# Performance work log

Hardware: AMD Instinct MI355X
Metric: run time of the kernel (lower is better)

The kernel has to match this reference:

```python
import jax, jax.numpy as jnp
import numpy as np

B, S, H, N = 2, 2048, 512, 64


def setup_inputs() -> dict:
    key = jax.random.key(0)
    ks = jax.random.split(key, 8)
    da_input = jax.random.normal(ks[0], (B, S, H), dtype=jnp.float32)
    # per-(batch, timestep) scalar time step; kept >= 4 so exp(delta*A) is stable
    da_orky_delta = jax.random.uniform(ks[1], (B, S), dtype=jnp.float32, minval=4.0, maxval=5.0)
    # all-negative A so the elementwise exp(delta*A) recurrence stays bounded
    A = -(jnp.abs(jax.random.normal(ks[2], (N, N), dtype=jnp.float32)) * 0.5 + 2.0)
    B_w = jax.random.normal(ks[3], (N, H), dtype=jnp.float32) * (1.0 / np.sqrt(H))
    C_w = jax.random.normal(ks[4], (H, N), dtype=jnp.float32) * (1.0 / np.sqrt(N))
    C_b = jax.random.normal(ks[5], (H,), dtype=jnp.float32) * 0.01
    D_w = jax.random.normal(ks[6], (H, H), dtype=jnp.float32) * (1.0 / np.sqrt(H))
    D_b = jax.random.normal(ks[7], (H,), dtype=jnp.float32) * 0.01
    return {"da_input": da_input, "da_orky_delta": da_orky_delta,
            "A": A, "B_w": B_w, "C_w": C_w, "C_b": C_b, "D_w": D_w, "D_b": D_b}


def _ssm_forward(da_input, da_orky_delta, A, B_w, C_w, C_b, D_w, D_b):
    Bsz, Slen, Hdim = da_input.shape
    Ndim = A.shape[0]
    # --- discretization: A_bar = exp(delta * A) (elementwise, as in torch.exp)
    A_bar = jnp.exp(da_orky_delta[:, :, None, None] * A)          # (B,S,N,N)
    I = jnp.eye(Ndim, dtype=A.dtype)
    A_inv = jnp.linalg.inv(A)                                      # (N,N)
    # B_bar = (A_bar - I) @ A^{-1} @ B_w  -> (B,S,N,H)
    B_bar = jnp.einsum('bsmn,nk,kh->bsmh', A_bar - I, A_inv, B_w)
    # per-step input projection: x_t @ B_bar_t^T  -> (B,S,N)
    inp_proj = jnp.einsum('bsh,bsnh->bsn', da_input, B_bar)

    # --- sequential selective scan: h_t = h_{t-1} @ A_bar_t + u_t
    def step(h, xs):
        Abar_t, u_t = xs                                           # (B,N,N), (B,N)
        h = jnp.einsum('bm,bmn->bn', h, Abar_t) + u_t
        return h, h

    h0 = jnp.zeros((Bsz, Ndim), dtype=da_input.dtype)
    _, hs = jax.lax.scan(step, h0, (jnp.swapaxes(A_bar, 0, 1), jnp.swapaxes(inp_proj, 0, 1)))
    hs = jnp.swapaxes(hs, 0, 1)                                    # (B,S,N)

    # y_t = C(h_t) + D(x_t)
    y = (jnp.einsum('bsn,hn->bsh', hs, C_w) + C_b
         + jnp.einsum('bsh,gh->bsg', da_input, D_w) + D_b)
    return y


def reference(da_input, da_orky_delta, A, B_w, C_w, C_b, D_w, D_b):
    return _ssm_forward(da_input, da_orky_delta, A, B_w, C_w, C_b, D_w, D_b)
```

## Files before the change

### kernel.cpp

```cpp
#include <hip/hip_runtime.h>
#include <hip/hip_bf16.h>

#define BSZ 2
#define SLEN 2048
#define HDIM 512
#define NDIM 64
#define TTOT (BSZ * SLEN)

#define CHUNK_L 4
#define HALO_K 3

typedef short bf16x8 __attribute__((ext_vector_type(8)));
typedef unsigned short u16x8 __attribute__((ext_vector_type(8)));
typedef float f32x4 __attribute__((ext_vector_type(4)));

__device__ inline unsigned short f2b(float f) {
    unsigned u = __float_as_uint(f);
    return (unsigned short)((u + 0x7FFFu + ((u >> 16) & 1u)) >> 16);
}
__device__ inline float b2f(unsigned short b) {
    return __uint_as_float(((unsigned)b) << 16);
}

__global__ __launch_bounds__(256) void k_pre(const float* __restrict__ A,
                                             const float* __restrict__ X,
                                             const float* __restrict__ Dw,
                                             const float* __restrict__ Bw,
                                             const float* __restrict__ Cb,
                                             const float* __restrict__ Db,
                                             float* __restrict__ Ainv,
                                             unsigned short* __restrict__ Vws,
                                             float* __restrict__ Y) {
    __shared__ float colb0[2][64], colb1[2][64];
    __shared__ float4 rowb0[2][16], rowb1[2][16];
    __shared__ unsigned short Xs[64][72];
    __shared__ unsigned short Ws[64][72];

    if (blockIdx.x == 0) {
        const int tid = threadIdx.x;
        const int r = tid >> 2;
        const int c = tid & 3;

        float4 q0, q1, q2, q3;
        {
            const float4* A4 = (const float4*)(A + (size_t)r * 64 + c * 16);
            q0 = A4[0]; q1 = A4[1]; q2 = A4[2]; q3 = A4[3];
        }

        for (int kb = 0; kb < 32; ++kb) {
            const int k0 = 2 * kb, k1 = k0 + 1;
            const int par = kb & 1;
            if (c == (k0 >> 4)) {
                int sel2 = (k0 & 15) >> 1;
                float v0 = q0.x, v1 = q0.y;
                if (sel2 == 1) { v0 = q0.z; v1 = q0.w; }
                if (sel2 == 2) { v0 = q1.x; v1 = q1.y; }
                if (sel2 == 3) { v0 = q1.z; v1 = q1.w; }
                if (sel2 == 4) { v0 = q2.x; v1 = q2.y; }
                if (sel2 == 5) { v0 = q2.z; v1 = q2.w; }
                if (sel2 == 6) { v0 = q3.x; v1 = q3.y; }
                if (sel2 == 7) { v0 = q3.z; v1 = q3.w; }
                colb0[par][r] = v0; colb1[par][r] = v1;
            }
            if (r == k0) {
                rowb0[par][c * 4 + 0] = q0; rowb0[par][c * 4 + 1] = q1;
                rowb0[par][c * 4 + 2] = q2; rowb0[par][c * 4 + 3] = q3;
            }
            if (r == k1) {
                rowb1[par][c * 4 + 0] = q0; rowb1[par][c * 4 + 1] = q1;
                rowb1[par][c * 4 + 2] = q2; rowb1[par][c * 4 + 3] = q3;
            }
            __syncthreads();

            float a00 = colb0[par][k0], a01 = colb1[par][k0];
            float a10 = colb0[par][k1], a11 = colb1[par][k1];
            float idet = 1.0f / (a00 * a11 - a01 * a10);
            float d00 = a11 * idet, d01 = -a01 * idet;
            float d10 = -a10 * idet, d11 = a00 * idet;

            float f0 = colb0[par][r], f1 = colb1[par][r];
            bool isp0 = (r == k0), isp1 = (r == k1);
            float g0 = f0 * d00 + f1 * d10;
            float g1 = f0 * d01 + f1 * d11;
            float al0 = isp0 ? d00 : (isp1 ? d10 : -g0);
            float al1 = isp0 ? d01 : (isp1 ? d11 : -g1);
            float beta = (isp0 || isp1) ? 0.0f : 1.0f;

            float4 p0q0 = rowb0[par][c * 4 + 0], p0q1 = rowb0[par][c * 4 + 1];
            float4 p0q2 = rowb0[par][c * 4 + 2], p0q3 = rowb0[par][c * 4 + 3];
            float4 p1q0 = rowb1[par][c * 4 + 0], p1q1 = rowb1[par][c * 4 + 1];
            float4 p1q2 = rowb1[par][c * 4 + 2], p1q3 = rowb1[par][c * 4 + 3];
            int selk = k0 - c * 16;

            #define UPD2(Q, P0, P1) { \
                float4 mv = q##Q; \
                float4 nv; \
                nv.x = fmaf(al0, P0.x, fmaf(al1, P1.x, beta * mv.x)); \
                nv.y = fmaf(al0, P0.y, fmaf(al1, P1.y, beta * mv.y)); \
                nv.z = fmaf(al0, P0.z, fmaf(al1, P1.z, beta * mv.z)); \
                nv.w = fmaf(al0, P0.w, fmaf(al1, P1.w, beta * mv.w)); \
                if (4 * (Q) + 0 == selk) { nv.x = al0; nv.y = al1; } \
                if (4 * (Q) + 2 == selk) { nv.z = al0; nv.w = al1; } \
                q##Q = nv; \
            }
            UPD2(0, p0q0, p1q0)
            UPD2(1, p0q1, p1q1)
            UPD2(2, p0q2, p1q2)
            UPD2(3, p0q3, p1q3)
        }

        float4* O = (float4*)(Ainv + (size_t)r * 64 + c * 16);
        O[0] = q0; O[1] = q1; O[2] = q2; O[3] = q3;
        return;
    }

    int tid = threadIdx.x;
    int wv = tid >> 6, lane = tid & 63;
    int sr = tid >> 2;
    int sc = (tid & 3) * 16;
    const int arow = wv * 16 + (lane & 15);
    const int akof = (lane >> 4) * 8;

    if (blockIdx.x <= 512) {
        int bid = blockIdx.x - 1;
        int t0 = (bid >> 3) * 64, h0 = (bid & 7) * 64;

        f32x4 acc0 = {0.f, 0.f, 0.f, 0.f}, acc1 = acc0, acc2 = acc0, acc3 = acc0;

        for (int st = 0; st < 8; ++st) {
            int k0 = st * 64;
            __syncthreads();
            {
                const float4* xp = (const float4*)&X[(size_t)(t0 + sr) * 512 + k0 + sc];
                const float4* wp = (const float4*)&Dw[(size_t)(h0 + sr) * 512 + k0 + sc];
                float4 x0 = xp[0], x1 = xp[1], x2 = xp[2], x3 = xp[3];
                float4 w0 = wp[0], w1 = wp[1], w2 = wp[2], w3 = wp[3];
                u16x8 a0 = {f2b(x0.x), f2b(x0.y), f2b(x0.z), f2b(x0.w),
                            f2b(x1.x), f2b(x1.y), f2b(x1.z), f2b(x1.w)};
                u16x8 a1 = {f2b(x2.x), f2b(x2.y), f2b(x2.z), f2b(x2.w),
                            f2b(x3.x), f2b(x3.y), f2b(x3.z), f2b(x3.w)};
                u16x8 b0 = {f2b(w0.x), f2b(w0.y), f2b(w0.z), f2b(w0.w),
                            f2b(w1.x), f2b(w1.y), f2b(w1.z), f2b(w1.w)};
                u16x8 b1 = {f2b(w2.x), f2b(w2.y), f2b(w2.z), f2b(w2.w),
                            f2b(w3.x), f2b(w3.y), f2b(w3.z), f2b(w3.w)};
                *(u16x8*)&Xs[sr][sc] = a0; *(u16x8*)&Xs[sr][sc + 8] = a1;
                *(u16x8*)&Ws[sr][sc] = b0; *(u16x8*)&Ws[sr][sc + 8] = b1;
            }
            __syncthreads();
            #pragma unroll
            for (int ks = 0; ks < 2; ++ks) {
                bf16x8 a = *(const bf16x8*)&Xs[arow][ks * 32 + akof];
                bf16x8 b0 = *(const bf16x8*)&Ws[0 * 16 + (lane & 15)][ks * 32 + akof];
                bf16x8 b1 = *(const bf16x8*)&Ws[1 * 16 + (lane & 15)][ks * 32 + akof];
                bf16x8 b2 = *(const bf16x8*)&Ws[2 * 16 + (lane & 15)][ks * 32 + akof];
                bf16x8 b3 = *(const bf16x8*)&Ws[3 * 16 + (lane & 15)][ks * 32 + akof];
                acc0 = __builtin_amdgcn_mfma_f32_16x16x32_bf16(a, b0, acc0, 0, 0, 0);
                acc1 = __builtin_amdgcn_mfma_f32_16x16x32_bf16(a, b1, acc1, 0, 0, 0);
                acc2 = __builtin_amdgcn_mfma_f32_16x16x32_bf16(a, b2, acc2, 0, 0, 0);
                acc3 = __builtin_amdgcn_mfma_f32_16x16x32_bf16(a, b3, acc3, 0, 0, 0);
            }
        }

        int rbase = t0 + wv * 16 + (lane >> 4) * 4;
        #define EPI(f, accv) { \
            int col = h0 + (f) * 16 + (lane & 15); \
            float bias = Cb[col] + Db[col]; \
            Y[(size_t)(rbase + 0) * 512 + col] = accv[0] + bias; \
            Y[(size_t)(rbase + 1) * 512 + col] = accv[1] + bias; \
            Y[(size_t)(rbase + 2) * 512 + col] = accv[2] + bias; \
            Y[(size_t)(rbase + 3) * 512 + col] = accv[3] + bias; \
        }
        EPI(0, acc0) EPI(1, acc1) EPI(2, acc2) EPI(3, acc3)
        return;
    }

    {
        int bidv = blockIdx.x - 513;
        int t0 = bidv * 64;

        f32x4 acc0 = {0.f, 0.f, 0.f, 0.f}, acc1 = acc0, acc2 = acc0, acc3 = acc0;

        for (int st = 0; st < 8; ++st) {
            int k0 = st * 64;
            __syncthreads();
            {
                const float4* xp = (const float4*)&X[(size_t)(t0 + sr) * 512 + k0 + sc];
                const float4* bp = (const float4*)&Bw[(size_t)sr * 512 + k0 + sc];
                float4 x0 = xp[0], x1 = xp[1], x2 = xp[2], x3 = xp[3];
                float4 w0 = bp[0], w1 = bp[1], w2 = bp[2], w3 = bp[3];
                u16x8 a0 = {f2b(x0.x), f2b(x0.y), f2b(x0.z), f2b(x0.w),
                            f2b(x1.x), f2b(x1.y), f2b(x1.z), f2b(x1.w)};
                u16x8 a1 = {f2b(x2.x), f2b(x2.y), f2b(x2.z), f2b(x2.w),
                            f2b(x3.x), f2b(x3.y), f2b(x3.z), f2b(x3.w)};
                u16x8 b0 = {f2b(w0.x), f2b(w0.y), f2b(w0.z), f2b(w0.w),
                            f2b(w1.x), f2b(w1.y), f2b(w1.z), f2b(w1.w)};
                u16x8 b1 = {f2b(w2.x), f2b(w2.y), f2b(w2.z), f2b(w2.w),
                            f2b(w3.x), f2b(w3.y), f2b(w3.z), f2b(w3.w)};
                *(u16x8*)&Xs[sr][sc] = a0; *(u16x8*)&Xs[sr][sc + 8] = a1;
                *(u16x8*)&Ws[sr][sc] = b0; *(u16x8*)&Ws[sr][sc + 8] = b1;
            }
            __syncthreads();
            #pragma unroll
            for (int ks = 0; ks < 2; ++ks) {
                bf16x8 a = *(const bf16x8*)&Xs[arow][ks * 32 + akof];
                bf16x8 b0 = *(const bf16x8*)&Ws[0 * 16 + (lane & 15)][ks * 32 + akof];
                bf16x8 b1 = *(const bf16x8*)&Ws[1 * 16 + (lane & 15)][ks * 32 + akof];
                bf16x8 b2 = *(const bf16x8*)&Ws[2 * 16 + (lane & 15)][ks * 32 + akof];
                bf16x8 b3 = *(const bf16x8*)&Ws[3 * 16 + (lane & 15)][ks * 32 + akof];
                acc0 = __builtin_amdgcn_mfma_f32_16x16x32_bf16(a, b0, acc0, 0, 0, 0);
                acc1 = __builtin_amdgcn_mfma_f32_16x16x32_bf16(a, b1, acc1, 0, 0, 0);
                acc2 = __builtin_amdgcn_mfma_f32_16x16x32_bf16(a, b2, acc2, 0, 0, 0);
                acc3 = __builtin_amdgcn_mfma_f32_16x16x32_bf16(a, b3, acc3, 0, 0, 0);
            }
        }

        int rbase = t0 + wv * 16 + (lane >> 4) * 4;
        #define EPIV(f, accv) { \
            int col = (f) * 16 + (lane & 15); \
            Vws[(size_t)(rbase + 0) * 64 + col] = f2b(accv[0]); \
            Vws[(size_t)(rbase + 1) * 64 + col] = f2b(accv[1]); \
            Vws[(size_t)(rbase + 2) * 64 + col] = f2b(accv[2]); \
            Vws[(size_t)(rbase + 3) * 64 + col] = f2b(accv[3]); \
        }
        EPIV(0, acc0) EPIV(1, acc1) EPIV(2, acc2) EPIV(3, acc3)
    }
}

__global__ __launch_bounds__(256) void k_rest(const unsigned short* __restrict__ Vws,
                                              const float* __restrict__ Ainv,
                                              const float* __restrict__ A,
                                              const float* __restrict__ delta,
                                              const float* __restrict__ Cw,
                                              float* __restrict__ Y) {
    __shared__ float As[64][68];
    __shared__ unsigned short Bs[64][72];
    __shared__ unsigned short Vs[20][72];
    __shared__ float Wls[20][68];
    __shared__ float Us[20][68];
    __shared__ float hb[4][64];
    __shared__ float dls[20];
    __shared__ unsigned short Hb[16][72];

    int tid = threadIdx.x;
    int wv = tid >> 6, lane = tid & 63;
    int t0 = blockIdx.x * 16;
    int b = t0 / SLEN;
    int s0 = t0 % SLEN;

    for (int e = tid; e < 4096; e += 256) As[e >> 6][e & 63] = A[e];
    {
        int sr = tid >> 2, sc4 = (tid & 3) * 16;
        const float4* ap = (const float4*)&Ainv[(size_t)sr * 64 + sc4];
        float4 a0 = ap[0], a1 = ap[1], a2 = ap[2], a3 = ap[3];
        u16x8 b0 = {f2b(a0.x), f2b(a0.y), f2b(a0.z), f2b(a0.w),
                    f2b(a1.x), f2b(a1.y), f2b(a1.z), f2b(a1.w)};
        u16x8 b1 = {f2b(a2.x), f2b(a2.y), f2b(a2.z), f2b(a2.w),
                    f2b(a3.x), f2b(a3.y), f2b(a3.z), f2b(a3.w)};
        *(u16x8*)&Bs[sr][sc4] = b0; *(u16x8*)&Bs[sr][sc4 + 8] = b1;
    }
    for (int e = tid; e < 19 * 8; e += 256) {
        int i = e >> 3, g = e & 7;
        int s = s0 - 3 + i;
        u16x8 v = {0, 0, 0, 0, 0, 0, 0, 0};
        if (s >= 0)
            v = *(const u16x8*)&Vws[(size_t)(b * SLEN + s) * 64 + g * 8];
        *(u16x8*)&Vs[i][g * 8] = v;
    }
    if (tid < 19) {
        int s = s0 - 3 + tid;
        dls[tid] = (s >= 0) ? delta[b * SLEN + s] : 0.0f;
    }
    __syncthreads();

    {
        const int n0 = wv * 16;
        const int arow = 3 + (lane & 15);
        const int akof = (lane >> 4) * 8;
        f32x4 acc = {0.f, 0.f, 0.f, 0.f};
        #pragma unroll
        for (int ks = 0; ks < 2; ++ks) {
            bf16x8 av = *(const bf16x8*)&Vs[arow][ks * 32 + akof];
            bf16x8 bv = *(const bf16x8*)&Bs[n0 + (lane & 15)][ks * 32 + akof];
            acc = __builtin_amdgcn_mfma_f32_16x16x32_bf16(av, bv, acc, 0, 0, 0);
        }
        #pragma unroll
        for (int i = 0; i < 4; ++i)
            Wls[3 + (lane >> 4) * 4 + i][n0 + (lane & 15)] = acc[i];
    }
    if (tid < 192) {
        int hr = tid >> 6;
        int n = tid & 63;
        float acc = 0.f;
        #pragma unroll 16
        for (int kk = 0; kk < 64; ++kk)
            acc = fmaf(b2f(Vs[hr][kk]), b2f(Bs[n][kk]), acc);
        Wls[hr][n] = acc;
    }
    __syncthreads();

    {
        float ar[64];
        #pragma unroll
        for (int q = 0; q < 16; ++q) {
            float4 v = *(const float4*)&As[lane][4 * q];
            ar[4 * q + 0] = v.x; ar[4 * q + 1] = v.y;
            ar[4 * q + 2] = v.z; ar[4 * q + 3] = v.w;
        }
        for (int i = wv; i < 19; i += 4) {
            float d = dls[i];
            float wn = Wls[i][lane];
            float p0 = 0.f, p1 = 0.f, p2 = 0.f, p3 = 0.f;
            #pragma unroll
            for (int q = 0; q < 16; ++q) {
                float4 vv = *(const float4*)&Wls[i][4 * q];
                p0 = fmaf(__expf(d * ar[4 * q + 0]), vv.x, p0);
                p1 = fmaf(__expf(d * ar[4 * q + 1]), vv.y, p1);
                p2 = fmaf(__expf(d * ar[4 * q + 2]), vv.z, p2);
                p3 = fmaf(__expf(d * ar[4 * q + 3]), vv.w, p3);
            }
            Us[i][lane] = ((p0 + p1) + (p2 + p3)) - wn;
        }
    }
    __syncthreads();

    {
        float ac[64];
        #pragma unroll
        for (int m = 0; m < 64; ++m) ac[m] = As[m][lane];
        hb[wv][lane] = 0.0f;
        __syncthreads();

        for (int st = 0; st < 7; ++st) {
            int j = wv * 4 + st;
            bool valid = (s0 - 3 + j) >= 0;
            float hn = 0.0f;
            if (valid) {
                float d = dls[j];
                hn = Us[j][lane];
                const float4* h4 = (const float4*)&hb[wv][0];
                #pragma unroll
                for (int q = 0; q < 16; ++q) {
                    float4 hv = h4[q];
                    hn = fmaf(__expf(d * ac[4 * q + 0]), hv.x, hn);
                    hn = fmaf(__expf(d * ac[4 * q + 1]), hv.y, hn);
                    hn = fmaf(__expf(d * ac[4 * q + 2]), hv.z, hn);
                    hn = fmaf(__expf(d * ac[4 * q + 3]), hv.w, hn);
                }
            }
            __syncthreads();
            if (valid) hb[wv][lane] = hn;
            __syncthreads();
            if (valid && st >= 3) Hb[j - 3][lane] = f2b(hn);
        }
    }
    __syncthreads();

    {
        const int tr = lane & 15;
        const int akof2 = (lane >> 4) * 8;
        f32x4 y0 = {0.f, 0.f, 0.f, 0.f}, y1 = y0, y2 = y0, y3 = y0;
        f32x4 y4 = y0, y5 = y0, y6 = y0, y7 = y0;
        #pragma unroll
        for (int ks = 0; ks < 2; ++ks) {
            bf16x8 av = *(const bf16x8*)&Hb[tr][ks * 32 + akof2];
            #define LDC(f, nm) \
                u16x8 nm##u; { \
                    const float4* cp = (const float4*)&Cw[ \
                        (size_t)(wv * 128 + (f) * 16 + tr) * 64 + ks * 32 + akof2]; \
                    float4 ca = cp[0], cb2 = cp[1]; \
                    nm##u = (u16x8){f2b(ca.x), f2b(ca.y), f2b(ca.z), f2b(ca.w), \
                                    f2b(cb2.x), f2b(cb2.y), f2b(cb2.z), f2b(cb2.w)}; \
                } \
                bf16x8 nm = *(bf16x8*)&nm##u;
            LDC(0, c0) LDC(1, c1) LDC(2, c2) LDC(3, c3)
            LDC(4, c4) LDC(5, c5) LDC(6, c6) LDC(7, c7)
            y0 = __builtin_amdgcn_mfma_f32_16x16x32_bf16(av, c0, y0, 0, 0, 0);
            y1 = __builtin_amdgcn_mfma_f32_16x16x32_bf16(av, c1, y1, 0, 0, 0);
            y2 = __builtin_amdgcn_mfma_f32_16x16x32_bf16(av, c2, y2, 0, 0, 0);
            y3 = __builtin_amdgcn_mfma_f32_16x16x32_bf16(av, c3, y3, 0, 0, 0);
            y4 = __builtin_amdgcn_mfma_f32_16x16x32_bf16(av, c4, y4, 0, 0, 0);
            y5 = __builtin_amdgcn_mfma_f32_16x16x32_bf16(av, c5, y5, 0, 0, 0);
            y6 = __builtin_amdgcn_mfma_f32_16x16x32_bf16(av, c6, y6, 0, 0, 0);
            y7 = __builtin_amdgcn_mfma_f32_16x16x32_bf16(av, c7, y7, 0, 0, 0);
        }
        int trow = (lane >> 4) * 4;
        #define EPIY(f, accv) { \
            int h = wv * 128 + (f) * 16 + (lane & 15); \
            Y[(size_t)(t0 + trow + 0) * 512 + h] += accv[0]; \
            Y[(size_t)(t0 + trow + 1) * 512 + h] += accv[1]; \
            Y[(size_t)(t0 + trow + 2) * 512 + h] += accv[2]; \
            Y[(size_t)(t0 + trow + 3) * 512 + h] += accv[3]; \
        }
        EPIY(0, y0) EPIY(1, y1) EPIY(2, y2) EPIY(3, y3)
        EPIY(4, y4) EPIY(5, y5) EPIY(6, y6) EPIY(7, y7)
    }
}

extern "C" void kernel_launch(void* const* d_in, const int* in_sizes, int n_in,
                              void* d_out, int out_size, void* d_ws, size_t ws_size,
                              hipStream_t stream) {
    const float* X     = (const float*)d_in[0];
    const float* delta = (const float*)d_in[1];
    const float* A     = (const float*)d_in[2];
    const float* Bw    = (const float*)d_in[3];
    const float* Cw    = (const float*)d_in[4];
    const float* Cb    = (const float*)d_in[5];
    const float* Dw    = (const float*)d_in[6];
    const float* Db    = (const float*)d_in[7];
    float* Y  = (float*)d_out;
    float* ws = (float*)d_ws;

    float* Ainv = ws;
    unsigned short* Vws = (unsigned short*)(ws + 4096);

    hipLaunchKernelGGL(k_pre, dim3(1 + 512 + TTOT / 64), dim3(256), 0, stream,
                       A, X, Dw, Bw, Cb, Db, Ainv, Vws, Y);
    hipLaunchKernelGGL(k_rest, dim3(TTOT / 16), dim3(256), 0, stream,
                       Vws, Ainv, A, delta, Cw, Y);
}
```

Before: 51.90 us.

## Fuse pre-pass and scan kernels into one cooperative kernel with grid sync

```diff
diff --git a/kernel.cpp b/kernel.cpp
--- a/kernel.cpp
+++ b/kernel.cpp
@@ -1,14 +1,14 @@
 #include <hip/hip_runtime.h>
 #include <hip/hip_bf16.h>
+#include <hip/hip_cooperative_groups.h>
+
+namespace cg = cooperative_groups;
 
 #define BSZ 2
 #define SLEN 2048
 #define HDIM 512
 #define NDIM 64
 #define TTOT (BSZ * SLEN)
-
-#define CHUNK_L 4
-#define HALO_K 3
 
 typedef short bf16x8 __attribute__((ext_vector_type(8)));
 typedef unsigned short u16x8 __attribute__((ext_vector_type(8)));
@@ -22,12 +22,14 @@
     return __uint_as_float(((unsigned)b) << 16);
 }
 
-__global__ __launch_bounds__(256) void k_pre(const float* __restrict__ A,
+__global__ __launch_bounds__(256) void k_all(const float* __restrict__ A,
                                              const float* __restrict__ X,
                                              const float* __restrict__ Dw,
                                              const float* __restrict__ Bw,
+                                             const float* __restrict__ Cw,
                                              const float* __restrict__ Cb,
                                              const float* __restrict__ Db,
+                                             const float* __restrict__ delta,
                                              float* __restrict__ Ainv,
                                              unsigned short* __restrict__ Vws,
                                              float* __restrict__ Y) {
@@ -35,10 +37,26 @@
     __shared__ float4 rowb0[2][16], rowb1[2][16];
     __shared__ unsigned short Xs[64][72];
     __shared__ unsigned short Ws[64][72];
+    __shared__ float As[64][68];
+    __shared__ unsigned short Bs[64][72];
+    __shared__ unsigned short Vs[20][72];
+    __shared__ float Wls[20][68];
+    __shared__ float Us[20][68];
+    __shared__ float hb[4][64];
+    __shared__ float dls[20];
+    __shared__ unsigned short Hb[16][72];
+
+    cg::grid_group grid = cg::this_grid();
+
+    int tid = threadIdx.x;
+    int wv = tid >> 6, lane = tid & 63;
+    int sr = tid >> 2;
+    int sc = (tid & 3) * 16;
+    const int arow = wv * 16 + (lane & 15);
+    const int akof = (lane >> 4) * 8;
 
     if (blockIdx.x == 0) {
-        const int tid = threadIdx.x;
-        const int r = tid >> 2;
+        const int r = sr;
         const int c = tid & 3;
 
         float4 q0, q1, q2, q3;
@@ -111,152 +129,119 @@
 
         float4* O = (float4*)(Ainv + (size_t)r * 64 + c * 16);
         O[0] = q0; O[1] = q1; O[2] = q2; O[3] = q3;
-        return;
-    }
-
-    int tid = threadIdx.x;
-    int wv = tid >> 6, lane = tid & 63;
-    int sr = tid >> 2;
-    int sc = (tid & 3) * 16;
-    const int arow = wv * 16 + (lane & 15);
-    const int akof = (lane >> 4) * 8;
-
-    if (blockIdx.x <= 512) {
-        int bid = blockIdx.x - 1;
-        int t0 = (bid >> 3) * 64, h0 = (bid & 7) * 64;
-
-        f32x4 acc0 = {0.f, 0.f, 0.f, 0.f}, acc1 = acc0, acc2 = acc0, acc3 = acc0;
-
-        for (int st = 0; st < 8; ++st) {
-            int k0 = st * 64;
-            __syncthreads();
-            {
-                const float4* xp = (const float4*)&X[(size_t)(t0 + sr) * 512 + k0 + sc];
-                const float4* wp = (const float4*)&Dw[(size_t)(h0 + sr) * 512 + k0 + sc];
-                float4 x0 = xp[0], x1 = xp[1], x2 = xp[2], x3 = xp[3];
-                float4 w0 = wp[0], w1 = wp[1], w2 = wp[2], w3 = wp[3];
-                u16x8 a0 = {f2b(x0.x), f2b(x0.y), f2b(x0.z), f2b(x0.w),
-                            f2b(x1.x), f2b(x1.y), f2b(x1.z), f2b(x1.w)};
-                u16x8 a1 = {f2b(x2.x), f2b(x2.y), f2b(x2.z), f2b(x2.w),
-                            f2b(x3.x), f2b(x3.y), f2b(x3.z), f2b(x3.w)};
-                u16x8 b0 = {f2b(w0.x), f2b(w0.y), f2b(w0.z), f2b(w0.w),
-                            f2b(w1.x), f2b(w1.y), f2b(w1.z), f2b(w1.w)};
-                u16x8 b1 = {f2b(w2.x), f2b(w2.y), f2b(w2.z), f2b(w2.w),
-                            f2b(w3.x), f2b(w3.y), f2b(w3.z), f2b(w3.w)};
-                *(u16x8*)&Xs[sr][sc] = a0; *(u16x8*)&Xs[sr][sc + 8] = a1;
-                *(u16x8*)&Ws[sr][sc] = b0; *(u16x8*)&Ws[sr][sc + 8] = b1;
-            }
-            __syncthreads();
-            #pragma unroll
-            for (int ks = 0; ks < 2; ++ks) {
-                bf16x8 a = *(const bf16x8*)&Xs[arow][ks * 32 + akof];
-                bf16x8 b0 = *(const bf16x8*)&Ws[0 * 16 + (lane & 15)][ks * 32 + akof];
-                bf16x8 b1 = *(const bf16x8*)&Ws[1 * 16 + (lane & 15)][ks * 32 + akof];
-                bf16x8 b2 = *(const bf16x8*)&Ws[2 * 16 + (lane & 15)][ks * 32 + akof];
-                bf16x8 b3 = *(const bf16x8*)&Ws[3 * 16 + (lane & 15)][ks * 32 + akof];
-                acc0 = __builtin_amdgcn_mfma_f32_16x16x32_bf16(a, b0, acc0, 0, 0, 0);
-                acc1 = __builtin_amdgcn_mfma_f32_16x16x32_bf16(a, b1, acc1, 0, 0, 0);
-                acc2 = __builtin_amdgcn_mfma_f32_16x16x32_bf16(a, b2, acc2, 0, 0, 0);
-                acc3 = __builtin_amdgcn_mfma_f32_16x16x32_bf16(a, b3, acc3, 0, 0, 0);
-            }
-        }
-
-        int rbase = t0 + wv * 16 + (lane >> 4) * 4;
-        #define EPI(f, accv) { \
-            int col = h0 + (f) * 16 + (lane & 15); \
-            float bias = Cb[col] + Db[col]; \
-            Y[(size_t)(rbase + 0) * 512 + col] = accv[0] + bias; \
-            Y[(size_t)(rbase + 1) * 512 + col] = accv[1] + bias; \
-            Y[(size_t)(rbase + 2) * 512 + col] = accv[2] + bias; \
-            Y[(size_t)(rbase + 3) * 512 + col] = accv[3] + bias; \
-        }
-        EPI(0, acc0) EPI(1, acc1) EPI(2, acc2) EPI(3, acc3)
-        return;
-    }
-
-    {
-        int bidv = blockIdx.x - 513;
-        int t0 = bidv * 64;
-
-        f32x4 acc0 = {0.f, 0.f, 0.f, 0.f}, acc1 = acc0, acc2 = acc0, acc3 = acc0;
-
-        for (int st = 0; st < 8; ++st) {
-            int k0 = st * 64;
-            __syncthreads();
-            {
-                const float4* xp = (const float4*)&X[(size_t)(t0 + sr) * 512 + k0 + sc];
-                const float4* bp = (const float4*)&Bw[(size_t)sr * 512 + k0 + sc];
-                float4 x0 = xp[0], x1 = xp[1], x2 = xp[2], x3 = xp[3];
-                float4 w0 = bp[0], w1 = bp[1], w2 = bp[2], w3 = bp[3];
-                u16x8 a0 = {f2b(x0.x), f2b(x0.y), f2b(x0.z), f2b(x0.w),
-                            f2b(x1.x), f2b(x1.y), f2b(x1.z), f2b(x1.w)};
-                u16x8 a1 = {f2b(x2.x), f2b(x2.y), f2b(x2.z), f2b(x2.w),
-                            f2b(x3.x), f2b(x3.y), f2b(x3.z), f2b(x3.w)};
-                u16x8 b0 = {f2b(w0.x), f2b(w0.y), f2b(w0.z), f2b(w0.w),
-                            f2b(w1.x), f2b(w1.y), f2b(w1.z), f2b(w1.w)};
-                u16x8 b1 = {f2b(w2.x), f2b(w2.y), f2b(w2.z), f2b(w2.w),
-                            f2b(w3.x), f2b(w3.y), f2b(w3.z), f2b(w3.w)};
-                *(u16x8*)&Xs[sr][sc] = a0; *(u16x8*)&Xs[sr][sc + 8] = a1;
-                *(u16x8*)&Ws[sr][sc] = b0; *(u16x8*)&Ws[sr][sc + 8] = b1;
-            }
-            __syncthreads();
-            #pragma unroll
-            for (int ks = 0; ks < 2; ++ks) {
-                bf16x8 a = *(const bf16x8*)&Xs[arow][ks * 32 + akof];
-                bf16x8 b0 = *(const bf16x8*)&Ws[0 * 16 + (lane & 15)][ks * 32 + akof];
-                bf16x8 b1 = *(const bf16x8*)&Ws[1 * 16 + (lane & 15)][ks * 32 + akof];
-                bf16x8 b2 = *(const bf16x8*)&Ws[2 * 16 + (lane & 15)][ks * 32 + akof];
-                bf16x8 b3 = *(const bf16x8*)&Ws[3 * 16 + (lane & 15)][ks * 32 + akof];
-                acc0 = __builtin_amdgcn_mfma_f32_16x16x32_bf16(a, b0, acc0, 0, 0, 0);
-                acc1 = __builtin_amdgcn_mfma_f32_16x16x32_bf16(a, b1, acc1, 0, 0, 0);
-                acc2 = __builtin_amdgcn_mfma_f32_16x16x32_bf16(a, b2, acc2, 0, 0, 0);
-                acc3 = __builtin_amdgcn_mfma_f32_16x16x32_bf16(a, b3, acc3, 0, 0, 0);
-            }
-        }
-
-        int rbase = t0 + wv * 16 + (lane >> 4) * 4;
-        #define EPIV(f, accv) { \
-            int col = (f) * 16 + (lane & 15); \
-            Vws[(size_t)(rbase + 0) * 64 + col] = f2b(accv[0]); \
-            Vws[(size_t)(rbase + 1) * 64 + col] = f2b(accv[1]); \
-            Vws[(size_t)(rbase + 2) * 64 + col] = f2b(accv[2]); \
-            Vws[(size_t)(rbase + 3) * 64 + col] = f2b(accv[3]); \
-        }
-        EPIV(0, acc0) EPIV(1, acc1) EPIV(2, acc2) EPIV(3, acc3)
-    }
-}
-
-__global__ __launch_bounds__(256) void k_rest(const unsigned short* __restrict__ Vws,
-                                              const float* __restrict__ Ainv,
-                                              const float* __restrict__ A,
-                                              const float* __restrict__ delta,
-                                              const float* __restrict__ Cw,
-                                              float* __restrict__ Y) {
-    __shared__ float As[64][68];
-    __shared__ unsigned short Bs[64][72];
-    __shared__ unsigned short Vs[20][72];
-    __shared__ float Wls[20][68];
-    __shared__ float Us[20][68];
-    __shared__ float hb[4][64];
-    __shared__ float dls[20];
-    __shared__ unsigned short Hb[16][72];
-
-    int tid = threadIdx.x;
-    int wv = tid >> 6, lane = tid & 63;
+    } else {
+        for (int tix = (int)blockIdx.x - 1; tix < 576; tix += 255) {
+            if (tix < 512) {
+                int t0 = (tix >> 3) * 64, h0 = (tix & 7) * 64;
+                f32x4 acc0 = {0.f, 0.f, 0.f, 0.f}, acc1 = acc0, acc2 = acc0, acc3 = acc0;
+                for (int st = 0; st < 8; ++st) {
+                    int k0 = st * 64;
+                    __syncthreads();
+                    {
+                        const float4* xp = (const float4*)&X[(size_t)(t0 + sr) * 512 + k0 + sc];
+                        const float4* wp = (const float4*)&Dw[(size_t)(h0 + sr) * 512 + k0 + sc];
+                        float4 x0 = xp[0], x1 = xp[1], x2 = xp[2], x3 = xp[3];
+                        float4 w0 = wp[0], w1 = wp[1], w2 = wp[2], w3 = wp[3];
+                        u16x8 a0 = {f2b(x0.x), f2b(x0.y), f2b(x0.z), f2b(x0.w),
+                                    f2b(x1.x), f2b(x1.y), f2b(x1.z), f2b(x1.w)};
+                        u16x8 a1 = {f2b(x2.x), f2b(x2.y), f2b(x2.z), f2b(x2.w),
+                                    f2b(x3.x), f2b(x3.y), f2b(x3.z), f2b(x3.w)};
+                        u16x8 b0 = {f2b(w0.x), f2b(w0.y), f2b(w0.z), f2b(w0.w),
+                                    f2b(w1.x), f2b(w1.y), f2b(w1.z), f2b(w1.w)};
+                        u16x8 b1 = {f2b(w2.x), f2b(w2.y), f2b(w2.z), f2b(w2.w),
+                                    f2b(w3.x), f2b(w3.y), f2b(w3.z), f2b(w3.w)};
+                        *(u16x8*)&Xs[sr][sc] = a0; *(u16x8*)&Xs[sr][sc + 8] = a1;
+                        *(u16x8*)&Ws[sr][sc] = b0; *(u16x8*)&Ws[sr][sc + 8] = b1;
+                    }
+                    __syncthreads();
+                    #pragma unroll
+                    for (int ks = 0; ks < 2; ++ks) {
+                        bf16x8 a = *(const bf16x8*)&Xs[arow][ks * 32 + akof];
+                        bf16x8 b0 = *(const bf16x8*)&Ws[0 * 16 + (lane & 15)][ks * 32 + akof];
+                        bf16x8 b1 = *(const bf16x8*)&Ws[1 * 16 + (lane & 15)][ks * 32 + akof];
+                        bf16x8 b2 = *(const bf16x8*)&Ws[2 * 16 + (lane & 15)][ks * 32 + akof];
+                        bf16x8 b3 = *(const bf16x8*)&Ws[3 * 16 + (lane & 15)][ks * 32 + akof];
+                        acc0 = __builtin_amdgcn_mfma_f32_16x16x32_bf16(a, b0, acc0, 0, 0, 0);
+                        acc1 = __builtin_amdgcn_mfma_f32_16x16x32_bf16(a, b1, acc1, 0, 0, 0);
+                        acc2 = __builtin_amdgcn_mfma_f32_16x16x32_bf16(a, b2, acc2, 0, 0, 0);
+                        acc3 = __builtin_amdgcn_mfma_f32_16x16x32_bf16(a, b3, acc3, 0, 0, 0);
+                    }
+                }
+                int rbase = t0 + wv * 16 + (lane >> 4) * 4;
+                #define EPI(f, accv) { \
+                    int col = h0 + (f) * 16 + (lane & 15); \
+                    float bias = Cb[col] + Db[col]; \
+                    Y[(size_t)(rbase + 0) * 512 + col] = accv[0] + bias; \
+                    Y[(size_t)(rbase + 1) * 512 + col] = accv[1] + bias; \
+                    Y[(size_t)(rbase + 2) * 512 + col] = accv[2] + bias; \
+                    Y[(size_t)(rbase + 3) * 512 + col] = accv[3] + bias; \
+                }
+                EPI(0, acc0) EPI(1, acc1) EPI(2, acc2) EPI(3, acc3)
+            } else {
+                int t0 = (tix - 512) * 64;
+                f32x4 acc0 = {0.f, 0.f, 0.f, 0.f}, acc1 = acc0, acc2 = acc0, acc3 = acc0;
+                for (int st = 0; st < 8; ++st) {
+                    int k0 = st * 64;
+                    __syncthreads();
+                    {
+                        const float4* xp = (const float4*)&X[(size_t)(t0 + sr) * 512 + k0 + sc];
+                        const float4* bp = (const float4*)&Bw[(size_t)sr * 512 + k0 + sc];
+                        float4 x0 = xp[0], x1 = xp[1], x2 = xp[2], x3 = xp[3];
+                        float4 w0 = bp[0], w1 = bp[1], w2 = bp[2], w3 = bp[3];
+                        u16x8 a0 = {f2b(x0.x), f2b(x0.y), f2b(x0.z), f2b(x0.w),
+                                    f2b(x1.x), f2b(x1.y), f2b(x1.z), f2b(x1.w)};
+                        u16x8 a1 = {f2b(x2.x), f2b(x2.y), f2b(x2.z), f2b(x2.w),
+                                    f2b(x3.x), f2b(x3.y), f2b(x3.z), f2b(x3.w)};
+                        u16x8 b0 = {f2b(w0.x), f2b(w0.y), f2b(w0.z), f2b(w0.w),
+                                    f2b(w1.x), f2b(w1.y), f2b(w1.z), f2b(w1.w)};
+                        u16x8 b1 = {f2b(w2.x), f2b(w2.y), f2b(w2.z), f2b(w2.w),
+                                    f2b(w3.x), f2b(w3.y), f2b(w3.z), f2b(w3.w)};
+                        *(u16x8*)&Xs[sr][sc] = a0; *(u16x8*)&Xs[sr][sc + 8] = a1;
+                        *(u16x8*)&Ws[sr][sc] = b0; *(u16x8*)&Ws[sr][sc + 8] = b1;
+                    }
+                    __syncthreads();
+                    #pragma unroll
+                    for (int ks = 0; ks < 2; ++ks) {
+                        bf16x8 a = *(const bf16x8*)&Xs[arow][ks * 32 + akof];
+                        bf16x8 b0 = *(const bf16x8*)&Ws[0 * 16 + (lane & 15)][ks * 32 + akof];
+                        bf16x8 b1 = *(const bf16x8*)&Ws[1 * 16 + (lane & 15)][ks * 32 + akof];
+                        bf16x8 b2 = *(const bf16x8*)&Ws[2 * 16 + (lane & 15)][ks * 32 + akof];
+                        bf16x8 b3 = *(const bf16x8*)&Ws[3 * 16 + (lane & 15)][ks * 32 + akof];
+                        acc0 = __builtin_amdgcn_mfma_f32_16x16x32_bf16(a, b0, acc0, 0, 0, 0);
+                        acc1 = __builtin_amdgcn_mfma_f32_16x16x32_bf16(a, b1, acc1, 0, 0, 0);
+                        acc2 = __builtin_amdgcn_mfma_f32_16x16x32_bf16(a, b2, acc2, 0, 0, 0);
+                        acc3 = __builtin_amdgcn_mfma_f32_16x16x32_bf16(a, b3, acc3, 0, 0, 0);
+                    }
+                }
+                int rbase = t0 + wv * 16 + (lane >> 4) * 4;
+                #define EPIV(f, accv) { \
+                    int col = (f) * 16 + (lane & 15); \
+                    Vws[(size_t)(rbase + 0) * 64 + col] = f2b(accv[0]); \
+                    Vws[(size_t)(rbase + 1) * 64 + col] = f2b(accv[1]); \
+                    Vws[(size_t)(rbase + 2) * 64 + col] = f2b(accv[2]); \
+                    Vws[(size_t)(rbase + 3) * 64 + col] = f2b(accv[3]); \
+                }
+                EPIV(0, acc0) EPIV(1, acc1) EPIV(2, acc2) EPIV(3, acc3)
+            }
+        }
+    }
+
+    grid.sync();
+
     int t0 = blockIdx.x * 16;
     int b = t0 / SLEN;
     int s0 = t0 % SLEN;
 
     for (int e = tid; e < 4096; e += 256) As[e >> 6][e & 63] = A[e];
     {
-        int sr = tid >> 2, sc4 = (tid & 3) * 16;
-        const float4* ap = (const float4*)&Ainv[(size_t)sr * 64 + sc4];
+        int sr2 = tid >> 2, sc4 = (tid & 3) * 16;
+        const float4* ap = (const float4*)&Ainv[(size_t)sr2 * 64 + sc4];
         float4 a0 = ap[0], a1 = ap[1], a2 = ap[2], a3 = ap[3];
         u16x8 b0 = {f2b(a0.x), f2b(a0.y), f2b(a0.z), f2b(a0.w),
                     f2b(a1.x), f2b(a1.y), f2b(a1.z), f2b(a1.w)};
         u16x8 b1 = {f2b(a2.x), f2b(a2.y), f2b(a2.z), f2b(a2.w),
                     f2b(a3.x), f2b(a3.y), f2b(a3.z), f2b(a3.w)};
-        *(u16x8*)&Bs[sr][sc4] = b0; *(u16x8*)&Bs[sr][sc4 + 8] = b1;
+        *(u16x8*)&Bs[sr2][sc4] = b0; *(u16x8*)&Bs[sr2][sc4 + 8] = b1;
     }
     for (int e = tid; e < 19 * 8; e += 256) {
         int i = e >> 3, g = e & 7;
@@ -274,12 +259,11 @@
 
     {
         const int n0 = wv * 16;
-        const int arow = 3 + (lane & 15);
-        const int akof = (lane >> 4) * 8;
+        const int ar2 = 3 + (lane & 15);
         f32x4 acc = {0.f, 0.f, 0.f, 0.f};
         #pragma unroll
         for (int ks = 0; ks < 2; ++ks) {
-            bf16x8 av = *(const bf16x8*)&Vs[arow][ks * 32 + akof];
+            bf16x8 av = *(const bf16x8*)&Vs[ar2][ks * 32 + akof];
             bf16x8 bv = *(const bf16x8*)&Bs[n0 + (lane & 15)][ks * 32 + akof];
             acc = __builtin_amdgcn_mfma_f32_16x16x32_bf16(av, bv, acc, 0, 0, 0);
         }
@@ -413,8 +397,9 @@
     float* Ainv = ws;
     unsigned short* Vws = (unsigned short*)(ws + 4096);
 
-    hipLaunchKernelGGL(k_pre, dim3(1 + 512 + TTOT / 64), dim3(256), 0, stream,
-                       A, X, Dw, Bw, Cb, Db, Ainv, Vws, Y);
-    hipLaunchKernelGGL(k_rest, dim3(TTOT / 16), dim3(256), 0, stream,
-                       Vws, Ainv, A, delta, Cw, Y);
+    void* args[] = {(void*)&A, (void*)&X, (void*)&Dw, (void*)&Bw, (void*)&Cw,
+                    (void*)&Cb, (void*)&Db, (void*)&delta,
+                    (void*)&Ainv, (void*)&Vws, (void*)&Y};
+    hipLaunchCooperativeKernel((const void*)k_all, dim3(256), dim3(256),
+                               args, 0, stream);
 }
```

New measurement: 101.1 us. +94.8%, slower.
